# Kernel optimization log

Hardware: AMD Instinct MI355X
Metric: run time of the kernel (lower is better)

## Reference

```python
import jax, jax.numpy as jnp
import numpy as np

BLOCKSIZE = 128
NUM_EXPERTS = 16
TOP_K = 6
HIDDEN = 2048
INTER = 1408
TOKENS = 4096
N_BLK_H = HIDDEN // BLOCKSIZE   # 16
N_BLK_I = -(-INTER // BLOCKSIZE)  # 11 (ceil)


def setup_inputs() -> dict:
    key = jax.random.key(0)
    ks = jax.random.split(key, 8)
    x = jax.random.normal(ks[0], (TOKENS, HIDDEN), dtype=jnp.float32)
    selected_experts = jax.random.randint(ks[1], (TOKENS, TOP_K), 0, NUM_EXPERTS)
    # quantized-style weights + per-block scales (dequant = w * repeat(s, blocksize))
    w0 = jax.random.normal(ks[2], (NUM_EXPERTS, INTER, HIDDEN), dtype=jnp.float32) * 0.02
    s0 = jax.random.uniform(ks[3], (NUM_EXPERTS, INTER, N_BLK_H), dtype=jnp.float32, minval=0.5, maxval=1.5)
    w1 = jax.random.normal(ks[4], (NUM_EXPERTS, INTER, HIDDEN), dtype=jnp.float32) * 0.02
    s1 = jax.random.uniform(ks[5], (NUM_EXPERTS, INTER, N_BLK_H), dtype=jnp.float32, minval=0.5, maxval=1.5)
    w2 = jax.random.normal(ks[6], (NUM_EXPERTS, HIDDEN, INTER), dtype=jnp.float32) * 0.02
    s2 = jax.random.uniform(ks[7], (NUM_EXPERTS, HIDDEN, N_BLK_I), dtype=jnp.float32, minval=0.5, maxval=1.5)
    return {"x": x, "selected_experts": selected_experts,
            "w0": w0, "s0": s0, "w1": w1, "s1": s1, "w2": w2, "s2": s2}


def _dequant(w, s):
    # w: [E, O, I], s: [E, O, ceil(I/bs)] -> broadcast each scale over its block
    s_full = jnp.repeat(s, BLOCKSIZE, axis=-1)[..., : w.shape[-1]]
    return w * s_full


def reference(x, selected_experts, w0, s0, w1, s1, w2, s2):
    # Dequantize block-quantized expert weights.
    W0 = _dequant(w0, s0)  # gate proj [E, I, H]
    W1 = _dequant(w1, s1)  # up proj   [E, I, H]
    W2 = _dequant(w2, s2)  # down proj [E, H, I]
    # Original loops token x slot, calling expert(x[i]). Equivalent batched form:
    # compute every expert on every token, then gather by (token, slot) index.
    gate = jnp.einsum('th,eih->eti', x, W0)            # [E, T, I]
    up = jnp.einsum('th,eih->eti', x, W1)              # [E, T, I]
    act = jax.nn.silu(gate) * up                       # [E, T, I]
    all_out = jnp.einsum('eti,ehi->eth', act, W2)      # [E, T, H]
    tok = jnp.arange(x.shape[0])[:, None]              # [T, 1]
    out = all_out[selected_experts, tok]               # [T, K, H]
    return out
```

## Files before the change

kernel.cpp:

```cpp
#include <hip/hip_runtime.h>
#include <stdint.h>

#define TOKENS 4096
#define HIDDEN 2048
#define INTER  1408
#define NEXP   16
#define TOPK   6
#define NPAIR  (TOKENS*TOPK)
#define BM     128
#define MAXTILES (NPAIR/BM + NEXP)
#define MAXT2  (NPAIR/256 + NEXP)
#define NT1    (INTER/128)
#define NT2    (HIDDEN/128)
#define NT2W   (HIDDEN/256)

typedef __attribute__((ext_vector_type(8))) short bf16x8;
typedef __attribute__((ext_vector_type(4))) float f32x4;

__device__ __forceinline__ short f2bf(float f){
  union { float f; uint32_t u; } v; v.f = f;
  uint32_t r = (v.u + 0x7FFFu + ((v.u >> 16) & 1u)) >> 16;
  return (short)(r & 0xFFFFu);
}

__device__ __forceinline__ void gld16(const void* g, const void* l){
  __builtin_amdgcn_global_load_lds((const __attribute__((address_space(1))) void*)g,
                                   (__attribute__((address_space(3))) void*)l, 16, 0, 0);
}

__device__ __forceinline__ f32x4 ntld4(const float* p){
  return __builtin_nontemporal_load((const f32x4*)p);
}

#define SB() __builtin_amdgcn_sched_barrier(0)
#define BAR() __builtin_amdgcn_s_barrier()
#define WAITV(n) asm volatile("s_waitcnt vmcnt(" #n ")" ::: "memory")
#define WAITL() asm volatile("s_waitcnt lgkmcnt(0)" ::: "memory")


__global__ void k_xcast(const float* __restrict__ x, short* __restrict__ xb){
  int i = (blockIdx.x * 256 + threadIdx.x) * 8;
  f32x4 a = ntld4(x + i);
  f32x4 b = ntld4(x + i + 4);
  bf16x8 o;
  #pragma unroll
  for (int j = 0; j < 4; ++j){ o[j] = f2bf(a[j]); o[4+j] = f2bf(b[j]); }
  *(bf16x8*)(xb + i) = o;
}

__global__ void k_deq01(const float* __restrict__ w0, const float* __restrict__ s0,
                        const float* __restrict__ w1, const float* __restrict__ s1,
                        short* __restrict__ o0, short* __restrict__ o1){
  int row = blockIdx.x;
  const float* w; const float* s; short* o;
  if (row < NEXP * INTER){ w = w0; s = s0; o = o0; }
  else { row -= NEXP * INTER; w = w1; s = s1; o = o1; }
  const size_t base = (size_t)row * HIDDEN;
  const int c = threadIdx.x * 8;
  float sc = s[(size_t)row * (HIDDEN/128) + (c >> 7)];
  f32x4 a = ntld4(w + base + c);
  f32x4 b = ntld4(w + base + c + 4);
  bf16x8 h;
  #pragma unroll
  for (int j = 0; j < 4; ++j){ h[j] = f2bf(a[j] * sc); h[4+j] = f2bf(b[j] * sc); }
  *(bf16x8*)(o + base + c) = h;
}

__global__ void k_deqw2(const float* __restrict__ w2, const float* __restrict__ s2,
                        short* __restrict__ o){
  const int total = NEXP * HIDDEN * (INTER / 8);
  for (int gi = blockIdx.x * 256 + threadIdx.x; gi < total; gi += gridDim.x * 256){
    int row = gi / (INTER / 8);
    int c = (gi - row * (INTER / 8)) * 8;
    const size_t base = (size_t)row * INTER;
    float sc = s2[(size_t)row * 11 + (c >> 7)];
    f32x4 a = ntld4(w2 + base + c);
    f32x4 b = ntld4(w2 + base + c + 4);
    bf16x8 h;
    #pragma unroll
    for (int j = 0; j < 4; ++j){ h[j] = f2bf(a[j] * sc); h[4+j] = f2bf(b[j] * sc); }
    *(bf16x8*)(o + base + c) = h;
  }
}

__global__ void k_dequant(const float* __restrict__ w, const float* __restrict__ s,
                          short* __restrict__ o, int rowlen, int nblk){
  const int row = blockIdx.x;
  const size_t base = (size_t)row * rowlen;
  for (int c = threadIdx.x * 8; c < rowlen; c += blockDim.x * 8){
    float sc = s[(size_t)row * nblk + (c >> 7)];
    f32x4 a = *(const f32x4*)(w + base + c);
    f32x4 b = *(const f32x4*)(w + base + c + 4);
    bf16x8 h;
    #pragma unroll
    for (int j = 0; j < 4; ++j){ h[j] = f2bf(a[j] * sc); h[4+j] = f2bf(b[j] * sc); }
    *(bf16x8*)(o + base + c) = h;
  }
}

__global__ void k_count(const int* __restrict__ sel, int* __restrict__ cnt){
  int p = blockIdx.x * 256 + threadIdx.x;
  if (p < NPAIR) atomicAdd(&cnt[sel[p]], 1);
}

__global__ void k_scan(const int* __restrict__ cnt, int* __restrict__ offsets,
                       int2* __restrict__ tiles, int* __restrict__ ntiles,
                       int2* __restrict__ tiles2, int* __restrict__ ntiles2){
  if (threadIdx.x != 0) return;
  int off = 0, nt = 0, nt2 = 0;
  for (int e = 0; e < NEXP; ++e){
    offsets[e] = off;
    int c = cnt[e];
    for (int m = 0; m < c; m += BM){
      int rows = c - m; if (rows > BM) rows = BM;
      tiles[nt++] = make_int2(off + m, (e << 16) | rows);
    }
    for (int m = 0; m < c; m += 256){
      int rows = c - m; if (rows > 256) rows = 256;
      tiles2[nt2++] = make_int2(off + m, (e << 16) | rows);
    }
    off += c;
  }
  offsets[NEXP] = off;
  *ntiles = nt;
  *ntiles2 = nt2;
}

__global__ void k_scatter(const int* __restrict__ sel, const int* __restrict__ offsets,
                          int* __restrict__ cursor, int* __restrict__ pair_tk){
  int p = blockIdx.x * 256 + threadIdx.x;
  if (p >= NPAIR) return;
  int e = sel[p];
  int pos = offsets[e] + atomicAdd(&cursor[e], 1);
  pair_tk[pos] = (p / TOPK) * 8 + (p % TOPK);
}


__global__ __launch_bounds__(512) void k_g1(
    const short* __restrict__ xb,
    const short* __restrict__ w0b, const short* __restrict__ w1b,
    const int2* __restrict__ tiles2, const int* __restrict__ ntiles2,
    const int* __restrict__ pair_tk, short* __restrict__ act)
{
  const int nwg = MAXT2 * NT1;
  const int orig = (int)(blockIdx.y * MAXT2 + blockIdx.x);
  const int wg = (orig & 7) * (nwg >> 3) + (orig >> 3);
  const int tx = wg % MAXT2, ty = wg / MAXT2;
  if (tx >= *ntiles2) return;
  const int2 td = tiles2[tx];
  const int mstart = td.x;
  const int e  = td.y >> 16;
  const int vr = td.y & 0xFFFF;

  __shared__ short lA[4][8192];
  __shared__ short lB[4][8192];

  const int tid = threadIdx.x, w = tid >> 6, lane = tid & 63;

  const short* pA[2]; const short* pB[2]; int sg8[2];
  #pragma unroll
  for (int i = 0; i < 2; ++i){
    int s = (w * 2 + i) * 64 + lane;
    int r = s >> 2, j = (s & 3) ^ ((s >> 3) & 3);
    sg8[i] = s * 8;
    int p = mstart + r; if (p >= NPAIR) p = NPAIR - 1;
    pA[i] = xb + (size_t)(pair_tk[p] >> 3) * HIDDEN + j * 8;
    int G = r >> 4, srow = (G >> 1) * 16 + (r & 15);
    const short* wsrc = (G & 1) ? w1b : w0b;
    pB[i] = wsrc + ((size_t)e * INTER + (size_t)ty * 128 + srow) * HIDDEN + j * 8;
  }
  auto stage = [&](int slot, int ko){
    #pragma unroll
    for (int i = 0; i < 2; ++i) gld16(pA[i] + ko, &lA[slot][sg8[i]]);
    #pragma unroll
    for (int i = 0; i < 2; ++i) gld16(pB[i] + ko, &lB[slot][sg8[i]]);
  };

  f32x4 acc[4][8];
  #pragma unroll
  for (int i = 0; i < 4; ++i)
    #pragma unroll
    for (int j = 0; j < 8; ++j) acc[i][j] = (f32x4)0.f;

  const int cc = lane & 15, ks = lane >> 4;
  const int sx = (ks ^ ((cc >> 1) & 3)) * 8;
  const int wm = w >> 1, wn = w & 1;
  int arow[4], brow[8];
  #pragma unroll
  for (int mf = 0; mf < 4; ++mf) arow[mf] = (wm * 64 + mf * 16 + cc) * 32;
  #pragma unroll
  for (int nf = 0; nf < 8; ++nf) brow[nf] = (wn * 128 + nf * 16 + cc) * 32;

  stage(0, 0); stage(1, 32); stage(2, 64); stage(3, 96);

  #pragma unroll 1
  for (int t = 0; t < 32; ++t){
    const int b = t & 1;
    if (t == 0)      { WAITV(12); }
    else if (t < 31) { WAITV(8);  }
    else             { WAITV(4);  }
    SB(); BAR(); SB();
    {
      bf16x8 a0[4], bb[8];
      #pragma unroll
      for (int mf = 0; mf < 4; ++mf) a0[mf] = *(const bf16x8*)&lA[b*2][arow[mf] + sx];
      #pragma unroll
      for (int nf = 0; nf < 8; ++nf) bb[nf] = *(const bf16x8*)&lB[b*2][brow[nf] + sx];
      if (t >= 1 && t + 1 < 32) stage(((t+1)&1)*2 + 1, (t+1)*64 + 32);
      WAITL(); SB();
      __builtin_amdgcn_s_setprio(1);
      #pragma unroll
      for (int nf = 0; nf < 8; ++nf)
        #pragma unroll
        for (int mf = 0; mf < 4; ++mf)
          acc[mf][nf] = __builtin_amdgcn_mfma_f32_16x16x32_bf16(a0[mf], bb[nf], acc[mf][nf], 0, 0, 0);
      __builtin_amdgcn_s_setprio(0);
      SB(); BAR(); SB();
    }
    if (t < 31) { WAITV(8); } else { WAITV(0); }
    SB(); BAR(); SB();
    {
      bf16x8 a0[4], bb[8];
      #pragma unroll
      for (int mf = 0; mf < 4; ++mf) a0[mf] = *(const bf16x8*)&lA[b*2+1][arow[mf] + sx];
      #pragma unroll
      for (int nf = 0; nf < 8; ++nf) bb[nf] = *(const bf16x8*)&lB[b*2+1][brow[nf] + sx];
      if (t + 2 < 32) stage(b*2, (t+2)*64);
      WAITL(); SB();
      __builtin_amdgcn_s_setprio(1);
      #pragma unroll
      for (int nf = 0; nf < 8; ++nf)
        #pragma unroll
        for (int mf = 0; mf < 4; ++mf)
          acc[mf][nf] = __builtin_amdgcn_mfma_f32_16x16x32_bf16(a0[mf], bb[nf], acc[mf][nf], 0, 0, 0);
      __builtin_amdgcn_s_setprio(0);
      SB(); BAR(); SB();
    }
  }

  #pragma unroll
  for (int mf = 0; mf < 4; ++mf){
    #pragma unroll
    for (int j = 0; j < 4; ++j){
      int row = wm * 64 + mf * 16 + ks * 4 + j;
      if (row < vr){
        short* ar = act + (size_t)(mstart + row) * INTER + (size_t)ty * 128 + cc;
        #pragma unroll
        for (int q = 0; q < 4; ++q){
          float g = acc[mf][2*q][j], u = acc[mf][2*q+1][j];
          float a = g / (1.f + __expf(-g)) * u;
          ar[(wn * 4 + q) * 16] = f2bf(a);
        }
      }
    }
  }
}

__global__ __launch_bounds__(512) void k_g2(
    const short* __restrict__ act, const short* __restrict__ w2b,
    const int2* __restrict__ tiles2, const int* __restrict__ ntiles2,
    const int* __restrict__ pair_tk, float* __restrict__ out)
{
  const int nwg = MAXT2 * NT2W;
  const int orig = (int)(blockIdx.y * MAXT2 + blockIdx.x);
  const int wg = (orig & 7) * (nwg >> 3) + (orig >> 3);
  const int tx = wg % MAXT2, ty = wg / MAXT2;
  if (tx >= *ntiles2) return;
  const int2 td = tiles2[tx];
  const int mstart = td.x;
  const int e  = td.y >> 16;
  const int vr = td.y & 0xFFFF;

  __shared__ short lA[4][8192];
  __shared__ short lB[4][8192];

  const int tid = threadIdx.x, w = tid >> 6, lane = tid & 63;

  const short* pA[2]; const short* pB[2]; int sg8[2];
  #pragma unroll
  for (int i = 0; i < 2; ++i){
    int s = (w * 2 + i) * 64 + lane;
    int r = s >> 2, j = (s & 3) ^ ((s >> 3) & 3);
    sg8[i] = s * 8;
    int p = mstart + r; if (p >= NPAIR) p = NPAIR - 1;
    pA[i] = act + (size_t)p * INTER + j * 8;
    pB[i] = w2b + ((size_t)e * HIDDEN + (size_t)ty * 256 + r) * INTER + j * 8;
  }
  auto stage = [&](int slot, int ko){
    #pragma unroll
    for (int i = 0; i < 2; ++i) gld16(pA[i] + ko, &lA[slot][sg8[i]]);
    #pragma unroll
    for (int i = 0; i < 2; ++i) gld16(pB[i] + ko, &lB[slot][sg8[i]]);
  };

  f32x4 acc[4][8];
  #pragma unroll
  for (int i = 0; i < 4; ++i)
    #pragma unroll
    for (int j = 0; j < 8; ++j) acc[i][j] = (f32x4)0.f;

  const int cc = lane & 15, ks = lane >> 4;
  const int sx = (ks ^ ((cc >> 1) & 3)) * 8;
  const int wm = w >> 1, wn = w & 1;
  int arow[4], brow[8];
  #pragma unroll
  for (int mf = 0; mf < 4; ++mf) arow[mf] = (wm * 64 + mf * 16 + cc) * 32;
  #pragma unroll
  for (int nf = 0; nf < 8; ++nf) brow[nf] = (wn * 128 + nf * 16 + cc) * 32;

  stage(0, 0); stage(1, 32); stage(2, 64); stage(3, 96);

  #pragma unroll 1
  for (int t = 0; t < 22; ++t){
    const int b = t & 1;
    if (t == 0)      { WAITV(12); }
    else if (t < 21) { WAITV(8);  }
    else             { WAITV(4);  }
    SB(); BAR(); SB();
    {
      bf16x8 a0[4], bb[8];
      #pragma unroll
      for (int mf = 0; mf < 4; ++mf) a0[mf] = *(const bf16x8*)&lA[b*2][arow[mf] + sx];
      #pragma unroll
      for (int nf = 0; nf < 8; ++nf) bb[nf] = *(const bf16x8*)&lB[b*2][brow[nf] + sx];
      if (t >= 1 && t + 1 < 22) stage(((t+1)&1)*2 + 1, (t+1)*64 + 32);
      WAITL(); SB();
      __builtin_amdgcn_s_setprio(1);
      #pragma unroll
      for (int nf = 0; nf < 8; ++nf)
        #pragma unroll
        for (int mf = 0; mf < 4; ++mf)
          acc[mf][nf] = __builtin_amdgcn_mfma_f32_16x16x32_bf16(a0[mf], bb[nf], acc[mf][nf], 0, 0, 0);
      __builtin_amdgcn_s_setprio(0);
      SB(); BAR(); SB();
    }
    if (t < 21) { WAITV(8); } else { WAITV(0); }
    SB(); BAR(); SB();
    {
      bf16x8 a0[4], bb[8];
      #pragma unroll
      for (int mf = 0; mf < 4; ++mf) a0[mf] = *(const bf16x8*)&lA[b*2+1][arow[mf] + sx];
      #pragma unroll
      for (int nf = 0; nf < 8; ++nf) bb[nf] = *(const bf16x8*)&lB[b*2+1][brow[nf] + sx];
      if (t + 2 < 22) stage(b*2, (t+2)*64);
      WAITL(); SB();
      __builtin_amdgcn_s_setprio(1);
      #pragma unroll
      for (int nf = 0; nf < 8; ++nf)
        #pragma unroll
        for (int mf = 0; mf < 4; ++mf)
          acc[mf][nf] = __builtin_amdgcn_mfma_f32_16x16x32_bf16(a0[mf], bb[nf], acc[mf][nf], 0, 0, 0);
      __builtin_amdgcn_s_setprio(0);
      SB(); BAR(); SB();
    }
  }

  #pragma unroll
  for (int mf = 0; mf < 4; ++mf){
    #pragma unroll
    for (int j = 0; j < 4; ++j){
      int row = wm * 64 + mf * 16 + ks * 4 + j;
      if (row < vr){
        int ptk = pair_tk[mstart + row];
        float* orow = out + ((size_t)(ptk >> 3) * TOPK + (ptk & 7)) * HIDDEN
                      + (size_t)ty * 256 + wn * 128 + cc;
        #pragma unroll
        for (int nf = 0; nf < 8; ++nf)
          orow[nf * 16] = acc[mf][nf][j];
      }
    }
  }
}


__global__ __launch_bounds__(256) void k_gemm1(
    const short* __restrict__ xb,
    const float* __restrict__ w0, const float* __restrict__ s0,
    const float* __restrict__ w1, const float* __restrict__ s1,
    const int2* __restrict__ tiles, const int* __restrict__ ntiles,
    const int* __restrict__ pair_tk, short* __restrict__ act)
{
  if ((int)blockIdx.x >= *ntiles) return;
  const int2 td = tiles[blockIdx.x];
  const int mstart = td.x;
  const int e  = td.y >> 16;
  const int vr = td.y & 0xFFFF;
  const int tid = threadIdx.x;
  const int lane = tid & 63;

  __shared__ short lA[BM * 32];
  __shared__ short lB0[BM * 40];
  __shared__ short lB1[BM * 40];

  const int r0 = tid >> 2, r1 = 64 + (tid >> 2);
  const int seg = tid & 3;
  int p0 = mstart + r0; if (p0 >= NPAIR) p0 = NPAIR - 1;
  int p1 = mstart + r1; if (p1 >= NPAIR) p1 = NPAIR - 1;
  const short* arow0 = xb + (size_t)(pair_tk[p0] >> 3) * HIDDEN + (seg ^ ((r0 >> 1) & 3)) * 8;
  const short* arow1 = xb + (size_t)(pair_tk[p1] >> 3) * HIDDEN + (seg ^ ((r1 >> 1) & 3)) * 8;
  const short* ldsA0 = &lA[tid * 8];
  const short* ldsA1 = &lA[2048 + tid * 8];

  const int brow = tid >> 1, half = tid & 1;
  const int gbrow = blockIdx.y * BM + brow;
  const float* w0row = w0 + ((size_t)e * INTER + gbrow) * HIDDEN + half * 16;
  const float* w1row = w1 + ((size_t)e * INTER + gbrow) * HIDDEN + half * 16;
  const float* s0row = s0 + ((size_t)e * INTER + gbrow) * (HIDDEN / 128);
  const float* s1row = s1 + ((size_t)e * INTER + gbrow) * (HIDDEN / 128);
  short* lb0w = &lB0[brow * 40 + half * 16];
  short* lb1w = &lB1[brow * 40 + half * 16];

  f32x4 acc0[4][4], acc1[4][4];
  #pragma unroll
  for (int i = 0; i < 4; ++i)
    #pragma unroll
    for (int j = 0; j < 4; ++j){ acc0[i][j] = (f32x4)0.f; acc1[i][j] = (f32x4)0.f; }

  const int wm = tid >> 7, wn = (tid >> 6) & 1;
  const int cc = lane & 15, ks = lane >> 4;

  for (int kt = 0; kt < HIDDEN / 32; ++kt){
    gld16(arow0 + kt * 32, ldsA0);
    gld16(arow1 + kt * 32, ldsA1);
    {
      float sc = s0row[kt >> 2];
      const float* g = w0row + kt * 32;
      f32x4 q0 = *(const f32x4*)g,       q1 = *(const f32x4*)(g + 4),
            q2 = *(const f32x4*)(g + 8), q3 = *(const f32x4*)(g + 12);
      bf16x8 h0, h1;
      #pragma unroll
      for (int i = 0; i < 4; ++i){
        h0[i] = f2bf(q0[i] * sc); h0[4 + i] = f2bf(q1[i] * sc);
        h1[i] = f2bf(q2[i] * sc); h1[4 + i] = f2bf(q3[i] * sc);
      }
      *(bf16x8*)lb0w = h0; *(bf16x8*)(lb0w + 8) = h1;
    }
    {
      float sc = s1row[kt >> 2];
      const float* g = w1row + kt * 32;
      f32x4 q0 = *(const f32x4*)g,       q1 = *(const f32x4*)(g + 4),
            q2 = *(const f32x4*)(g + 8), q3 = *(const f32x4*)(g + 12);
      bf16x8 h0, h1;
      #pragma unroll
      for (int i = 0; i < 4; ++i){
        h0[i] = f2bf(q0[i] * sc); h0[4 + i] = f2bf(q1[i] * sc);
        h1[i] = f2bf(q2[i] * sc); h1[4 + i] = f2bf(q3[i] * sc);
      }
      *(bf16x8*)lb1w = h0; *(bf16x8*)(lb1w + 8) = h1;
    }
    __syncthreads();

    bf16x8 af[4];
    #pragma unroll
    for (int mf = 0; mf < 4; ++mf){
      int row = wm * 64 + mf * 16 + cc;
      af[mf] = *(const bf16x8*)&lA[row * 32 + ((ks ^ ((row >> 1) & 3)) * 8)];
    }
    #pragma unroll
    for (int nf = 0; nf < 4; ++nf){
      int rb = wn * 64 + nf * 16 + cc;
      bf16x8 b0 = *(const bf16x8*)&lB0[rb * 40 + ks * 8];
      bf16x8 b1 = *(const bf16x8*)&lB1[rb * 40 + ks * 8];
      #pragma unroll
      for (int mf = 0; mf < 4; ++mf)
        acc0[mf][nf] = __builtin_amdgcn_mfma_f32_16x16x32_bf16(af[mf], b0, acc0[mf][nf], 0, 0, 0);
      #pragma unroll
      for (int mf = 0; mf < 4; ++mf)
        acc1[mf][nf] = __builtin_amdgcn_mfma_f32_16x16x32_bf16(af[mf], b1, acc1[mf][nf], 0, 0, 0);
    }
    __syncthreads();
  }

  const int rbase = wm * 64 + (lane >> 4) * 4;
  #pragma unroll
  for (int mf = 0; mf < 4; ++mf){
    #pragma unroll
    for (int j = 0; j < 4; ++j){
      int row = rbase + mf * 16 + j;
      if (row < vr){
        short* ar = act + (size_t)(mstart + row) * INTER + blockIdx.y * BM + wn * 64 + cc;
        #pragma unroll
        for (int nf = 0; nf < 4; ++nf){
          float g = acc0[mf][nf][j], u = acc1[mf][nf][j];
          float a = g / (1.f + __expf(-g)) * u;
          ar[nf * 16] = f2bf(a);
        }
      }
    }
  }
}

__global__ __launch_bounds__(256) void k_gemm2(
    const short* __restrict__ act,
    const float* __restrict__ w2, const float* __restrict__ s2,
    const int2* __restrict__ tiles, const int* __restrict__ ntiles,
    const int* __restrict__ pair_tk, float* __restrict__ out)
{
  if ((int)blockIdx.x >= *ntiles) return;
  const int2 td = tiles[blockIdx.x];
  const int mstart = td.x;
  const int e  = td.y >> 16;
  const int vr = td.y & 0xFFFF;
  const int tid = threadIdx.x;
  const int lane = tid & 63;

  __shared__ short lA[BM * 32];
  __shared__ short lB[BM * 40];

  const int r0 = tid >> 2, r1 = 64 + (tid >> 2);
  const int seg = tid & 3;
  int p0 = mstart + r0; if (p0 >= NPAIR) p0 = NPAIR - 1;
  int p1 = mstart + r1; if (p1 >= NPAIR) p1 = NPAIR - 1;
  const short* arow0 = act + (size_t)p0 * INTER + (seg ^ ((r0 >> 1) & 3)) * 8;
  const short* arow1 = act + (size_t)p1 * INTER + (seg ^ ((r1 >> 1) & 3)) * 8;
  const short* ldsA0 = &lA[tid * 8];
  const short* ldsA1 = &lA[2048 + tid * 8];

  const int brow = tid >> 1, half = tid & 1;
  const int gbrow = blockIdx.y * BM + brow;
  const float* w2row = w2 + ((size_t)e * HIDDEN + gbrow) * INTER + half * 16;
  const float* s2row = s2 + ((size_t)e * HIDDEN + gbrow) * 11;
  short* lbw = &lB[brow * 40 + half * 16];

  f32x4 acc[4][4];
  #pragma unroll
  for (int i = 0; i < 4; ++i)
    #pragma unroll
    for (int j = 0; j < 4; ++j) acc[i][j] = (f32x4)0.f;

  const int wm = tid >> 7, wn = (tid >> 6) & 1;
  const int cc = lane & 15, ks = lane >> 4;

  for (int kt = 0; kt < INTER / 32; ++kt){
    gld16(arow0 + kt * 32, ldsA0);
    gld16(arow1 + kt * 32, ldsA1);
    {
      float sc = s2row[kt >> 2];
      const float* g = w2row + kt * 32;
      f32x4 q0 = *(const f32x4*)g,       q1 = *(const f32x4*)(g + 4),
            q2 = *(const f32x4*)(g + 8), q3 = *(const f32x4*)(g + 12);
      bf16x8 h0, h1;
      #pragma unroll
      for (int i = 0; i < 4; ++i){
        h0[i] = f2bf(q0[i] * sc); h0[4 + i] = f2bf(q1[i] * sc);
        h1[i] = f2bf(q2[i] * sc); h1[4 + i] = f2bf(q3[i] * sc);
      }
      *(bf16x8*)lbw = h0; *(bf16x8*)(lbw + 8) = h1;
    }
    __syncthreads();

    bf16x8 af[4];
    #pragma unroll
    for (int mf = 0; mf < 4; ++mf){
      int row = wm * 64 + mf * 16 + cc;
      af[mf] = *(const bf16x8*)&lA[row * 32 + ((ks ^ ((row >> 1) & 3)) * 8)];
    }
    #pragma unroll
    for (int nf = 0; nf < 4; ++nf){
      int rb = wn * 64 + nf * 16 + cc;
      bf16x8 b = *(const bf16x8*)&lB[rb * 40 + ks * 8];
      #pragma unroll
      for (int mf = 0; mf < 4; ++mf)
        acc[mf][nf] = __builtin_amdgcn_mfma_f32_16x16x32_bf16(af[mf], b, acc[mf][nf], 0, 0, 0);
    }
    __syncthreads();
  }

  const int rbase = wm * 64 + (lane >> 4) * 4;
  #pragma unroll
  for (int mf = 0; mf < 4; ++mf){
    #pragma unroll
    for (int j = 0; j < 4; ++j){
      int row = rbase + mf * 16 + j;
      if (row < vr){
        int ptk = pair_tk[mstart + row];
        float* orow = out + ((size_t)(ptk >> 3) * TOPK + (ptk & 7)) * HIDDEN
                      + blockIdx.y * BM + wn * 64 + cc;
        #pragma unroll
        for (int nf = 0; nf < 4; ++nf)
          orow[nf * 16] = acc[mf][nf][j];
      }
    }
  }
}


extern "C" void kernel_launch(void* const* d_in, const int* in_sizes, int n_in,
                              void* d_out, int out_size, void* d_ws, size_t ws_size,
                              hipStream_t stream)
{
  const float* x  = (const float*)d_in[0];
  const int*   sel= (const int*)  d_in[1];
  const float* w0 = (const float*)d_in[2];
  const float* s0 = (const float*)d_in[3];
  const float* w1 = (const float*)d_in[4];
  const float* s1 = (const float*)d_in[5];
  const float* w2 = (const float*)d_in[6];
  const float* s2 = (const float*)d_in[7];
  float* out = (float*)d_out;

  char* ws = (char*)d_ws;
  size_t o = 0;
  auto alloc = [&](size_t n){ size_t r = o; o = (o + n + 255) & ~(size_t)255; return r; };
  int*  cnt     = (int*) (ws + alloc(64));
  int*  cursor  = (int*) (ws + alloc(64));
  int*  offsets = (int*) (ws + alloc(68));
  int*  ntiles  = (int*) (ws + alloc(4));
  int*  ntiles2 = (int*) (ws + alloc(4));
  int2* tiles   = (int2*)(ws + alloc(MAXTILES * 8));
  int2* tiles2  = (int2*)(ws + alloc(MAXT2 * 8));
  int*  pair_tk = (int*) (ws + alloc((size_t)NPAIR * 4));
  short* xb     = (short*)(ws + alloc((size_t)TOKENS * HIDDEN * 2));
  short* act    = (short*)(ws + alloc((size_t)NPAIR * INTER * 2));
  const size_t WSZ = (size_t)NEXP * INTER * HIDDEN * 2;
  short* w0b    = (short*)(ws + alloc(WSZ));
  short* w1b    = (short*)(ws + alloc(WSZ));
  short* w2b    = (short*)(ws + alloc(WSZ));
  const bool predeq = (ws_size >= o);
  (void)in_sizes; (void)n_in; (void)out_size;

  hipMemsetAsync(ws, 0, 512, stream);

  k_xcast  <<<(TOKENS * HIDDEN) / (256 * 8), 256, 0, stream>>>(x, xb);
  k_count  <<<(NPAIR + 255) / 256, 256, 0, stream>>>(sel, cnt);
  k_scan   <<<1, 64, 0, stream>>>(cnt, offsets, tiles, ntiles, tiles2, ntiles2);
  k_scatter<<<(NPAIR + 255) / 256, 256, 0, stream>>>(sel, offsets, cursor, pair_tk);

  if (predeq){
    k_deq01<<<2 * NEXP * INTER, 256, 0, stream>>>(w0, s0, w1, s1, w0b, w1b);
    k_g1<<<dim3(MAXT2, NT1), 512, 0, stream>>>(xb, w0b, w1b,
                                               tiles2, ntiles2, pair_tk, act);
    k_deqw2<<<2048, 256, 0, stream>>>(w2, s2, w2b);
    k_g2<<<dim3(MAXT2, NT2W), 512, 0, stream>>>(act, w2b,
                                                tiles2, ntiles2, pair_tk, out);
  } else {
    k_gemm1<<<dim3(MAXTILES, NT1), 256, 0, stream>>>(xb, w0, s0, w1, s1,
                                                     tiles, ntiles, pair_tk, act);
    k_gemm2<<<dim3(MAXTILES, NT2), 256, 0, stream>>>(act, w2, s2,
                                                     tiles, ntiles, pair_tk, out);
  }
}
```

Measured before the change: 818.4 us.

## Switch GEMMs to 32x32x16 MFMA and fuse w2 dequant into first GEMM

Both grouped GEMM kernels move from 16x16x32 MFMA tiles to 32x32x16 MFMA with 16-float accumulators, and the LDS read addressing, swizzle and epilogue row mapping are adjusted to match. The gate/up interleave granularity in the B staging changes from 16 to 32 rows so the silu*up pairing lines up with the larger fragments. The separate w2 dequantization kernel is removed, and its grid-stride loop is appended to the tail of k_g1, so every workgroup, including early-exit ones, dequantizes part of w2 after its GEMM work. This saves a launch and lets memory-bound dequant overlap with compute-bound tiles, but it lengthens k_g1 and its tail and changes register pressure.

```diff
diff --git a/kernel.cpp b/kernel.cpp
--- a/kernel.cpp
+++ b/kernel.cpp
@@ -14,8 +14,9 @@
 #define NT2    (HIDDEN/128)
 #define NT2W   (HIDDEN/256)
 
-typedef __attribute__((ext_vector_type(8))) short bf16x8;
-typedef __attribute__((ext_vector_type(4))) float f32x4;
+typedef __attribute__((ext_vector_type(8)))  short bf16x8;
+typedef __attribute__((ext_vector_type(4)))  float f32x4;
+typedef __attribute__((ext_vector_type(16))) float f32x16;
 
 __device__ __forceinline__ short f2bf(float f){
   union { float f; uint32_t u; } v; v.f = f;
@@ -66,23 +67,6 @@
   *(bf16x8*)(o + base + c) = h;
 }
 
-__global__ void k_deqw2(const float* __restrict__ w2, const float* __restrict__ s2,
-                        short* __restrict__ o){
-  const int total = NEXP * HIDDEN * (INTER / 8);
-  for (int gi = blockIdx.x * 256 + threadIdx.x; gi < total; gi += gridDim.x * 256){
-    int row = gi / (INTER / 8);
-    int c = (gi - row * (INTER / 8)) * 8;
-    const size_t base = (size_t)row * INTER;
-    float sc = s2[(size_t)row * 11 + (c >> 7)];
-    f32x4 a = ntld4(w2 + base + c);
-    f32x4 b = ntld4(w2 + base + c + 4);
-    bf16x8 h;
-    #pragma unroll
-    for (int j = 0; j < 4; ++j){ h[j] = f2bf(a[j] * sc); h[4+j] = f2bf(b[j] * sc); }
-    *(bf16x8*)(o + base + c) = h;
-  }
-}
-
 __global__ void k_dequant(const float* __restrict__ w, const float* __restrict__ s,
                           short* __restrict__ o, int rowlen, int nblk){
   const int row = blockIdx.x;
@@ -140,118 +124,136 @@
     const short* __restrict__ xb,
     const short* __restrict__ w0b, const short* __restrict__ w1b,
     const int2* __restrict__ tiles2, const int* __restrict__ ntiles2,
-    const int* __restrict__ pair_tk, short* __restrict__ act)
+    const int* __restrict__ pair_tk, short* __restrict__ act,
+    const float* __restrict__ w2, const float* __restrict__ s2,
+    short* __restrict__ w2b)
 {
   const int nwg = MAXT2 * NT1;
   const int orig = (int)(blockIdx.y * MAXT2 + blockIdx.x);
   const int wg = (orig & 7) * (nwg >> 3) + (orig >> 3);
   const int tx = wg % MAXT2, ty = wg / MAXT2;
-  if (tx >= *ntiles2) return;
-  const int2 td = tiles2[tx];
-  const int mstart = td.x;
-  const int e  = td.y >> 16;
-  const int vr = td.y & 0xFFFF;
+  const int tid = threadIdx.x, w = tid >> 6, lane = tid & 63;
 
   __shared__ short lA[4][8192];
   __shared__ short lB[4][8192];
 
-  const int tid = threadIdx.x, w = tid >> 6, lane = tid & 63;
-
-  const short* pA[2]; const short* pB[2]; int sg8[2];
-  #pragma unroll
-  for (int i = 0; i < 2; ++i){
-    int s = (w * 2 + i) * 64 + lane;
-    int r = s >> 2, j = (s & 3) ^ ((s >> 3) & 3);
-    sg8[i] = s * 8;
-    int p = mstart + r; if (p >= NPAIR) p = NPAIR - 1;
-    pA[i] = xb + (size_t)(pair_tk[p] >> 3) * HIDDEN + j * 8;
-    int G = r >> 4, srow = (G >> 1) * 16 + (r & 15);
-    const short* wsrc = (G & 1) ? w1b : w0b;
-    pB[i] = wsrc + ((size_t)e * INTER + (size_t)ty * 128 + srow) * HIDDEN + j * 8;
-  }
-  auto stage = [&](int slot, int ko){
-    #pragma unroll
-    for (int i = 0; i < 2; ++i) gld16(pA[i] + ko, &lA[slot][sg8[i]]);
-    #pragma unroll
-    for (int i = 0; i < 2; ++i) gld16(pB[i] + ko, &lB[slot][sg8[i]]);
-  };
-
-  f32x4 acc[4][8];
-  #pragma unroll
-  for (int i = 0; i < 4; ++i)
-    #pragma unroll
-    for (int j = 0; j < 8; ++j) acc[i][j] = (f32x4)0.f;
-
-  const int cc = lane & 15, ks = lane >> 4;
-  const int sx = (ks ^ ((cc >> 1) & 3)) * 8;
-  const int wm = w >> 1, wn = w & 1;
-  int arow[4], brow[8];
-  #pragma unroll
-  for (int mf = 0; mf < 4; ++mf) arow[mf] = (wm * 64 + mf * 16 + cc) * 32;
-  #pragma unroll
-  for (int nf = 0; nf < 8; ++nf) brow[nf] = (wn * 128 + nf * 16 + cc) * 32;
-
-  stage(0, 0); stage(1, 32); stage(2, 64); stage(3, 96);
-
-  #pragma unroll 1
-  for (int t = 0; t < 32; ++t){
-    const int b = t & 1;
-    if (t == 0)      { WAITV(12); }
-    else if (t < 31) { WAITV(8);  }
-    else             { WAITV(4);  }
-    SB(); BAR(); SB();
-    {
-      bf16x8 a0[4], bb[8];
-      #pragma unroll
-      for (int mf = 0; mf < 4; ++mf) a0[mf] = *(const bf16x8*)&lA[b*2][arow[mf] + sx];
-      #pragma unroll
-      for (int nf = 0; nf < 8; ++nf) bb[nf] = *(const bf16x8*)&lB[b*2][brow[nf] + sx];
-      if (t >= 1 && t + 1 < 32) stage(((t+1)&1)*2 + 1, (t+1)*64 + 32);
-      WAITL(); SB();
-      __builtin_amdgcn_s_setprio(1);
-      #pragma unroll
-      for (int nf = 0; nf < 8; ++nf)
-        #pragma unroll
-        for (int mf = 0; mf < 4; ++mf)
-          acc[mf][nf] = __builtin_amdgcn_mfma_f32_16x16x32_bf16(a0[mf], bb[nf], acc[mf][nf], 0, 0, 0);
-      __builtin_amdgcn_s_setprio(0);
-      SB(); BAR(); SB();
-    }
-    if (t < 31) { WAITV(8); } else { WAITV(0); }
-    SB(); BAR(); SB();
-    {
-      bf16x8 a0[4], bb[8];
-      #pragma unroll
-      for (int mf = 0; mf < 4; ++mf) a0[mf] = *(const bf16x8*)&lA[b*2+1][arow[mf] + sx];
-      #pragma unroll
-      for (int nf = 0; nf < 8; ++nf) bb[nf] = *(const bf16x8*)&lB[b*2+1][brow[nf] + sx];
-      if (t + 2 < 32) stage(b*2, (t+2)*64);
-      WAITL(); SB();
-      __builtin_amdgcn_s_setprio(1);
-      #pragma unroll
-      for (int nf = 0; nf < 8; ++nf)
-        #pragma unroll
-        for (int mf = 0; mf < 4; ++mf)
-          acc[mf][nf] = __builtin_amdgcn_mfma_f32_16x16x32_bf16(a0[mf], bb[nf], acc[mf][nf], 0, 0, 0);
-      __builtin_amdgcn_s_setprio(0);
-      SB(); BAR(); SB();
-    }
-  }
-
-  #pragma unroll
-  for (int mf = 0; mf < 4; ++mf){
-    #pragma unroll
-    for (int j = 0; j < 4; ++j){
-      int row = wm * 64 + mf * 16 + ks * 4 + j;
-      if (row < vr){
-        short* ar = act + (size_t)(mstart + row) * INTER + (size_t)ty * 128 + cc;
-        #pragma unroll
-        for (int q = 0; q < 4; ++q){
-          float g = acc[mf][2*q][j], u = acc[mf][2*q+1][j];
-          float a = g / (1.f + __expf(-g)) * u;
-          ar[(wn * 4 + q) * 16] = f2bf(a);
+  if (tx < *ntiles2){
+    const int2 td = tiles2[tx];
+    const int mstart = td.x;
+    const int e  = td.y >> 16;
+    const int vr = td.y & 0xFFFF;
+
+    const short* pA[2]; const short* pB[2]; int sg8[2];
+    #pragma unroll
+    for (int i = 0; i < 2; ++i){
+      int s = (w * 2 + i) * 64 + lane;
+      int r = s >> 2, j = (s & 3) ^ ((s >> 3) & 3);
+      sg8[i] = s * 8;
+      int p = mstart + r; if (p >= NPAIR) p = NPAIR - 1;
+      pA[i] = xb + (size_t)(pair_tk[p] >> 3) * HIDDEN + j * 8;
+      int G = r >> 5, srow = (G >> 1) * 32 + (r & 31);
+      const short* wsrc = (G & 1) ? w1b : w0b;
+      pB[i] = wsrc + ((size_t)e * INTER + (size_t)ty * 128 + srow) * HIDDEN + j * 8;
+    }
+    auto stage = [&](int slot, int ko){
+      #pragma unroll
+      for (int i = 0; i < 2; ++i) gld16(pA[i] + ko, &lA[slot][sg8[i]]);
+      #pragma unroll
+      for (int i = 0; i < 2; ++i) gld16(pB[i] + ko, &lB[slot][sg8[i]]);
+    };
+
+    f32x16 acc[2][4];
+    #pragma unroll
+    for (int i = 0; i < 2; ++i)
+      #pragma unroll
+      for (int j = 0; j < 4; ++j) acc[i][j] = (f32x16)0.f;
+
+    const int c32 = lane & 31, kg = lane >> 5;
+    const int wm = w >> 1, wn = w & 1;
+    int arow[2], axor[2], brow[4], bxor[4];
+    #pragma unroll
+    for (int mf = 0; mf < 2; ++mf){
+      int r = wm * 64 + mf * 32 + c32;
+      arow[mf] = r * 32; axor[mf] = (r >> 1) & 3;
+    }
+    #pragma unroll
+    for (int nf = 0; nf < 4; ++nf){
+      int r = wn * 128 + nf * 32 + c32;
+      brow[nf] = r * 32; bxor[nf] = (r >> 1) & 3;
+    }
+
+    stage(0, 0); stage(1, 32); stage(2, 64); stage(3, 96);
+
+    #pragma unroll 1
+    for (int t = 0; t < 32; ++t){
+      const int b = t & 1;
+      #pragma unroll
+      for (int h = 0; h < 2; ++h){
+        if (t == 0 && h == 0)      { WAITV(12); }
+        else if (t < 31)           { WAITV(8);  }
+        else if (h == 0)           { WAITV(4);  }
+        else                       { WAITV(0);  }
+        SB(); BAR(); SB();
+        const short* A = lA[b*2 + h];
+        const short* B = lB[b*2 + h];
+        bf16x8 av[2][2], bv[4][2];
+        #pragma unroll
+        for (int mf = 0; mf < 2; ++mf)
+          #pragma unroll
+          for (int k2 = 0; k2 < 2; ++k2)
+            av[mf][k2] = *(const bf16x8*)&A[arow[mf] + (((k2*2+kg) ^ axor[mf]) * 8)];
+        #pragma unroll
+        for (int nf = 0; nf < 4; ++nf)
+          #pragma unroll
+          for (int k2 = 0; k2 < 2; ++k2)
+            bv[nf][k2] = *(const bf16x8*)&B[brow[nf] + (((k2*2+kg) ^ bxor[nf]) * 8)];
+        if (h == 0){ if (t >= 1 && t + 1 < 32) stage(((t+1)&1)*2 + 1, (t+1)*64 + 32); }
+        else       { if (t + 2 < 32)           stage(b*2, (t+2)*64); }
+        WAITL(); SB();
+        __builtin_amdgcn_s_setprio(1);
+        #pragma unroll
+        for (int k2 = 0; k2 < 2; ++k2)
+          #pragma unroll
+          for (int nf = 0; nf < 4; ++nf)
+            #pragma unroll
+            for (int mf = 0; mf < 2; ++mf)
+              acc[mf][nf] = __builtin_amdgcn_mfma_f32_32x32x16_bf16(av[mf][k2], bv[nf][k2], acc[mf][nf], 0, 0, 0);
+        __builtin_amdgcn_s_setprio(0);
+        SB(); BAR(); SB();
+      }
+    }
+
+    #pragma unroll
+    for (int mf = 0; mf < 2; ++mf){
+      #pragma unroll
+      for (int r = 0; r < 16; ++r){
+        int row = wm * 64 + mf * 32 + (r & 3) + 8 * (r >> 2) + 4 * kg;
+        if (row < vr){
+          short* ar = act + (size_t)(mstart + row) * INTER + (size_t)ty * 128 + c32;
+          #pragma unroll
+          for (int t2 = 0; t2 < 2; ++t2){
+            float g = acc[mf][2*t2][r], u = acc[mf][2*t2+1][r];
+            float a = g / (1.f + __expf(-g)) * u;
+            ar[(wn * 2 + t2) * 32] = f2bf(a);
+          }
         }
       }
+    }
+  }
+
+  {
+    const int total = NEXP * HIDDEN * (INTER / 8);
+    for (int gi = orig * 512 + tid; gi < total; gi += nwg * 512){
+      int row = gi / (INTER / 8);
+      int c = (gi - row * (INTER / 8)) * 8;
+      const size_t base = (size_t)row * INTER;
+      float sc = s2[(size_t)row * 11 + (c >> 7)];
+      f32x4 a = ntld4(w2 + base + c);
+      f32x4 b = ntld4(w2 + base + c + 4);
+      bf16x8 h;
+      #pragma unroll
+      for (int j = 0; j < 4; ++j){ h[j] = f2bf(a[j] * sc); h[4+j] = f2bf(b[j] * sc); }
+      *(bf16x8*)(w2b + base + c) = h;
     }
   }
 }
@@ -293,80 +295,79 @@
     for (int i = 0; i < 2; ++i) gld16(pB[i] + ko, &lB[slot][sg8[i]]);
   };
 
-  f32x4 acc[4][8];
-  #pragma unroll
-  for (int i = 0; i < 4; ++i)
-    #pragma unroll
-    for (int j = 0; j < 8; ++j) acc[i][j] = (f32x4)0.f;
-
-  const int cc = lane & 15, ks = lane >> 4;
-  const int sx = (ks ^ ((cc >> 1) & 3)) * 8;
+  f32x16 acc[2][4];
+  #pragma unroll
+  for (int i = 0; i < 2; ++i)
+    #pragma unroll
+    for (int j = 0; j < 4; ++j) acc[i][j] = (f32x16)0.f;
+
+  const int c32 = lane & 31, kg = lane >> 5;
   const int wm = w >> 1, wn = w & 1;
-  int arow[4], brow[8];
-  #pragma unroll
-  for (int mf = 0; mf < 4; ++mf) arow[mf] = (wm * 64 + mf * 16 + cc) * 32;
-  #pragma unroll
-  for (int nf = 0; nf < 8; ++nf) brow[nf] = (wn * 128 + nf * 16 + cc) * 32;
+  int arow[2], axor[2], brow[4], bxor[4];
+  #pragma unroll
+  for (int mf = 0; mf < 2; ++mf){
+    int r = wm * 64 + mf * 32 + c32;
+    arow[mf] = r * 32; axor[mf] = (r >> 1) & 3;
+  }
+  #pragma unroll
+  for (int nf = 0; nf < 4; ++nf){
+    int r = wn * 128 + nf * 32 + c32;
+    brow[nf] = r * 32; bxor[nf] = (r >> 1) & 3;
+  }
 
   stage(0, 0); stage(1, 32); stage(2, 64); stage(3, 96);
 
   #pragma unroll 1
   for (int t = 0; t < 22; ++t){
     const int b = t & 1;
-    if (t == 0)      { WAITV(12); }
-    else if (t < 21) { WAITV(8);  }
-    else             { WAITV(4);  }
-    SB(); BAR(); SB();
-    {
-      bf16x8 a0[4], bb[8];
-      #pragma unroll
-      for (int mf = 0; mf < 4; ++mf) a0[mf] = *(const bf16x8*)&lA[b*2][arow[mf] + sx];
-      #pragma unroll
-      for (int nf = 0; nf < 8; ++nf) bb[nf] = *(const bf16x8*)&lB[b*2][brow[nf] + sx];
-      if (t >= 1 && t + 1 < 22) stage(((t+1)&1)*2 + 1, (t+1)*64 + 32);
+    #pragma unroll
+    for (int h = 0; h < 2; ++h){
+      if (t == 0 && h == 0)      { WAITV(12); }
+      else if (t < 21)           { WAITV(8);  }
+      else if (h == 0)           { WAITV(4);  }
+      else                       { WAITV(0);  }
+      SB(); BAR(); SB();
+      const short* A = lA[b*2 + h];
+      const short* B = lB[b*2 + h];
+      bf16x8 av[2][2], bv[4][2];
+      #pragma unroll
+      for (int mf = 0; mf < 2; ++mf)
+        #pragma unroll
+        for (int k2 = 0; k2 < 2; ++k2)
+          av[mf][k2] = *(const bf16x8*)&A[arow[mf] + (((k2*2+kg) ^ axor[mf]) * 8)];
+      #pragma unroll
+      for (int nf = 0; nf < 4; ++nf)
+        #pragma unroll
+        for (int k2 = 0; k2 < 2; ++k2)
+          bv[nf][k2] = *(const bf16x8*)&B[brow[nf] + (((k2*2+kg) ^ bxor[nf]) * 8)];
+      if (h == 0){ if (t >= 1 && t + 1 < 22) stage(((t+1)&1)*2 + 1, (t+1)*64 + 32); }
+      else       { if (t + 2 < 22)           stage(b*2, (t+2)*64); }
       WAITL(); SB();
       __builtin_amdgcn_s_setprio(1);
       #pragma unroll
-      for (int nf = 0; nf < 8; ++nf)
-        #pragma unroll
-        for (int mf = 0; mf < 4; ++mf)
-          acc[mf][nf] = __builtin_amdgcn_mfma_f32_16x16x32_bf16(a0[mf], bb[nf], acc[mf][nf], 0, 0, 0);
+      for (int k2 = 0; k2 < 2; ++k2)
+        #pragma unroll
+        for (int nf = 0; nf < 4; ++nf)
+          #pragma unroll
+          for (int mf = 0; mf < 2; ++mf)
+            acc[mf][nf] = __builtin_amdgcn_mfma_f32_32x32x16_bf16(av[mf][k2], bv[nf][k2], acc[mf][nf], 0, 0, 0);
       __builtin_amdgcn_s_setprio(0);
       SB(); BAR(); SB();
     }
-    if (t < 21) { WAITV(8); } else { WAITV(0); }
-    SB(); BAR(); SB();
-    {
-      bf16x8 a0[4], bb[8];
-      #pragma unroll
-      for (int mf = 0; mf < 4; ++mf) a0[mf] = *(const bf16x8*)&lA[b*2+1][arow[mf] + sx];
-      #pragma unroll
-      for (int nf = 0; nf < 8; ++nf) bb[nf] = *(const bf16x8*)&lB[b*2+1][brow[nf] + sx];
-      if (t + 2 < 22) stage(b*2, (t+2)*64);
-      WAITL(); SB();
-      __builtin_amdgcn_s_setprio(1);
-      #pragma unroll
-      for (int nf = 0; nf < 8; ++nf)
-        #pragma unroll
-        for (int mf = 0; mf < 4; ++mf)
-          acc[mf][nf] = __builtin_amdgcn_mfma_f32_16x16x32_bf16(a0[mf], bb[nf], acc[mf][nf], 0, 0, 0);
-      __builtin_amdgcn_s_setprio(0);
-      SB(); BAR(); SB();
-    }
-  }
-
-  #pragma unroll
-  for (int mf = 0; mf < 4; ++mf){
-    #pragma unroll
-    for (int j = 0; j < 4; ++j){
-      int row = wm * 64 + mf * 16 + ks * 4 + j;
+  }
+
+  #pragma unroll
+  for (int mf = 0; mf < 2; ++mf){
+    #pragma unroll
+    for (int r = 0; r < 16; ++r){
+      int row = wm * 64 + mf * 32 + (r & 3) + 8 * (r >> 2) + 4 * kg;
       if (row < vr){
         int ptk = pair_tk[mstart + row];
         float* orow = out + ((size_t)(ptk >> 3) * TOPK + (ptk & 7)) * HIDDEN
-                      + (size_t)ty * 256 + wn * 128 + cc;
-        #pragma unroll
-        for (int nf = 0; nf < 8; ++nf)
-          orow[nf * 16] = acc[mf][nf][j];
+                      + (size_t)ty * 256 + wn * 128 + c32;
+        #pragma unroll
+        for (int nf = 0; nf < 4; ++nf)
+          orow[nf * 32] = acc[mf][nf][r];
       }
     }
   }
@@ -629,8 +630,8 @@
   if (predeq){
     k_deq01<<<2 * NEXP * INTER, 256, 0, stream>>>(w0, s0, w1, s1, w0b, w1b);
     k_g1<<<dim3(MAXT2, NT1), 512, 0, stream>>>(xb, w0b, w1b,
-                                               tiles2, ntiles2, pair_tk, act);
-    k_deqw2<<<2048, 256, 0, stream>>>(w2, s2, w2b);
+                                               tiles2, ntiles2, pair_tk, act,
+                                               w2, s2, w2b);
     k_g2<<<dim3(MAXT2, NT2W), 512, 0, stream>>>(act, w2b,
                                                 tiles2, ntiles2, pair_tk, out);
   } else {
```

Result: slower. 863.3 us (+5.5%).

## Stage GEMM epilogues through LDS for coalesced stores and fuse x cast

Applied to the files above, without the earlier changes.

The epilogues of both grouped GEMMs now write accumulator fragments into shared memory first, then each wave stores whole rows contiguously (4-byte writes for the bf16 activations, 16-byte writes for the fp32 output). The old path issued scattered 2- and 4-byte strided stores. The x-to-bf16 cast is also folded into the w0/w1 dequant launch as extra blocks, removing one kernel launch. The cost is extra LDS traffic and barriers in the epilogue, and k_g2 needs two passes because its 256x256 fp32 tile does not fit in LDS at once.

```diff
diff --git a/kernel.cpp b/kernel.cpp
--- a/kernel.cpp
+++ b/kernel.cpp
@@ -38,20 +38,21 @@
 #define WAITL() asm volatile("s_waitcnt lgkmcnt(0)" ::: "memory")
 
 
-__global__ void k_xcast(const float* __restrict__ x, short* __restrict__ xb){
-  int i = (blockIdx.x * 256 + threadIdx.x) * 8;
-  f32x4 a = ntld4(x + i);
-  f32x4 b = ntld4(x + i + 4);
-  bf16x8 o;
-  #pragma unroll
-  for (int j = 0; j < 4; ++j){ o[j] = f2bf(a[j]); o[4+j] = f2bf(b[j]); }
-  *(bf16x8*)(xb + i) = o;
-}
-
-__global__ void k_deq01(const float* __restrict__ w0, const float* __restrict__ s0,
-                        const float* __restrict__ w1, const float* __restrict__ s1,
-                        short* __restrict__ o0, short* __restrict__ o1){
+__global__ void k_deq01x(const float* __restrict__ x, short* __restrict__ xb,
+                         const float* __restrict__ w0, const float* __restrict__ s0,
+                         const float* __restrict__ w1, const float* __restrict__ s1,
+                         short* __restrict__ o0, short* __restrict__ o1){
   int row = blockIdx.x;
+  if (row >= 2 * NEXP * INTER){
+    int i = ((row - 2 * NEXP * INTER) * 256 + threadIdx.x) * 8;
+    f32x4 a = ntld4(x + i);
+    f32x4 b = ntld4(x + i + 4);
+    bf16x8 o;
+    #pragma unroll
+    for (int j = 0; j < 4; ++j){ o[j] = f2bf(a[j]); o[4+j] = f2bf(b[j]); }
+    *(bf16x8*)(xb + i) = o;
+    return;
+  }
   const float* w; const float* s; short* o;
   if (row < NEXP * INTER){ w = w0; s = s0; o = o0; }
   else { row -= NEXP * INTER; w = w1; s = s1; o = o1; }
@@ -83,19 +84,14 @@
   }
 }
 
-__global__ void k_dequant(const float* __restrict__ w, const float* __restrict__ s,
-                          short* __restrict__ o, int rowlen, int nblk){
-  const int row = blockIdx.x;
-  const size_t base = (size_t)row * rowlen;
-  for (int c = threadIdx.x * 8; c < rowlen; c += blockDim.x * 8){
-    float sc = s[(size_t)row * nblk + (c >> 7)];
-    f32x4 a = *(const f32x4*)(w + base + c);
-    f32x4 b = *(const f32x4*)(w + base + c + 4);
-    bf16x8 h;
-    #pragma unroll
-    for (int j = 0; j < 4; ++j){ h[j] = f2bf(a[j] * sc); h[4+j] = f2bf(b[j] * sc); }
-    *(bf16x8*)(o + base + c) = h;
-  }
+__global__ void k_xcast(const float* __restrict__ x, short* __restrict__ xb){
+  int i = (blockIdx.x * 256 + threadIdx.x) * 8;
+  f32x4 a = ntld4(x + i);
+  f32x4 b = ntld4(x + i + 4);
+  bf16x8 o;
+  #pragma unroll
+  for (int j = 0; j < 4; ++j){ o[j] = f2bf(a[j]); o[4+j] = f2bf(b[j]); }
+  *(bf16x8*)(xb + i) = o;
 }
 
 __global__ void k_count(const int* __restrict__ sel, int* __restrict__ cnt){
@@ -152,8 +148,9 @@
   const int e  = td.y >> 16;
   const int vr = td.y & 0xFFFF;
 
-  __shared__ short lA[4][8192];
-  __shared__ short lB[4][8192];
+  __shared__ short lmem[8][8192];
+  short (*lA)[8192] = lmem;
+  short (*lB)[8192] = lmem + 4;
 
   const int tid = threadIdx.x, w = tid >> 6, lane = tid & 63;
 
@@ -238,20 +235,28 @@
     }
   }
 
+  short* lT = (short*)lmem;
+  __syncthreads();
   #pragma unroll
   for (int mf = 0; mf < 4; ++mf){
     #pragma unroll
     for (int j = 0; j < 4; ++j){
       int row = wm * 64 + mf * 16 + ks * 4 + j;
-      if (row < vr){
-        short* ar = act + (size_t)(mstart + row) * INTER + (size_t)ty * 128 + cc;
-        #pragma unroll
-        for (int q = 0; q < 4; ++q){
-          float g = acc[mf][2*q][j], u = acc[mf][2*q+1][j];
-          float a = g / (1.f + __expf(-g)) * u;
-          ar[(wn * 4 + q) * 16] = f2bf(a);
-        }
-      }
+      #pragma unroll
+      for (int q = 0; q < 4; ++q){
+        float g = acc[mf][2*q][j], u = acc[mf][2*q+1][j];
+        float a = g / (1.f + __expf(-g)) * u;
+        lT[row * 128 + (wn * 4 + q) * 16 + cc] = f2bf(a);
+      }
+    }
+  }
+  __syncthreads();
+  #pragma unroll 1
+  for (int rr = 0; rr < 32; ++rr){
+    int row = w * 32 + rr;
+    if (row < vr){
+      uint32_t v = *(const uint32_t*)&lT[row * 128 + lane * 2];
+      *(uint32_t*)&act[(size_t)(mstart + row) * INTER + (size_t)ty * 128 + lane * 2] = v;
     }
   }
 }
@@ -271,8 +276,9 @@
   const int e  = td.y >> 16;
   const int vr = td.y & 0xFFFF;
 
-  __shared__ short lA[4][8192];
-  __shared__ short lB[4][8192];
+  __shared__ short lmem[8][8192];
+  short (*lA)[8192] = lmem;
+  short (*lB)[8192] = lmem + 4;
 
   const int tid = threadIdx.x, w = tid >> 6, lane = tid & 63;
 
@@ -355,18 +361,34 @@
     }
   }
 
-  #pragma unroll
-  for (int mf = 0; mf < 4; ++mf){
-    #pragma unroll
-    for (int j = 0; j < 4; ++j){
-      int row = wm * 64 + mf * 16 + ks * 4 + j;
+  float* lT = (float*)lmem;
+  #pragma unroll 1
+  for (int p = 0; p < 2; ++p){
+    __syncthreads();
+    if ((wm >> 1) == p){
+      int rb = (wm & 1) * 64;
+      #pragma unroll
+      for (int mf = 0; mf < 4; ++mf){
+        #pragma unroll
+        for (int j = 0; j < 4; ++j){
+          int prow = rb + mf * 16 + ks * 4 + j;
+          #pragma unroll
+          for (int nf = 0; nf < 8; ++nf)
+            lT[prow * 256 + wn * 128 + nf * 16 + cc] = acc[mf][nf][j];
+        }
+      }
+    }
+    __syncthreads();
+    #pragma unroll 1
+    for (int rr = 0; rr < 16; ++rr){
+      int prow = w * 16 + rr;
+      int row = p * 128 + prow;
       if (row < vr){
         int ptk = pair_tk[mstart + row];
         float* orow = out + ((size_t)(ptk >> 3) * TOPK + (ptk & 7)) * HIDDEN
-                      + (size_t)ty * 256 + wn * 128 + cc;
-        #pragma unroll
-        for (int nf = 0; nf < 8; ++nf)
-          orow[nf * 16] = acc[mf][nf][j];
+                      + (size_t)ty * 256;
+        f32x4 v = *(const f32x4*)&lT[prow * 256 + lane * 4];
+        *(f32x4*)&orow[lane * 4] = v;
       }
     }
   }
@@ -621,19 +643,20 @@
 
   hipMemsetAsync(ws, 0, 512, stream);
 
-  k_xcast  <<<(TOKENS * HIDDEN) / (256 * 8), 256, 0, stream>>>(x, xb);
   k_count  <<<(NPAIR + 255) / 256, 256, 0, stream>>>(sel, cnt);
   k_scan   <<<1, 64, 0, stream>>>(cnt, offsets, tiles, ntiles, tiles2, ntiles2);
   k_scatter<<<(NPAIR + 255) / 256, 256, 0, stream>>>(sel, offsets, cursor, pair_tk);
 
   if (predeq){
-    k_deq01<<<2 * NEXP * INTER, 256, 0, stream>>>(w0, s0, w1, s1, w0b, w1b);
+    k_deq01x<<<2 * NEXP * INTER + (TOKENS * HIDDEN) / (256 * 8), 256, 0, stream>>>(
+        x, xb, w0, s0, w1, s1, w0b, w1b);
     k_g1<<<dim3(MAXT2, NT1), 512, 0, stream>>>(xb, w0b, w1b,
                                                tiles2, ntiles2, pair_tk, act);
     k_deqw2<<<2048, 256, 0, stream>>>(w2, s2, w2b);
     k_g2<<<dim3(MAXT2, NT2W), 512, 0, stream>>>(act, w2b,
                                                 tiles2, ntiles2, pair_tk, out);
   } else {
+    k_xcast  <<<(TOKENS * HIDDEN) / (256 * 8), 256, 0, stream>>>(x, xb);
     k_gemm1<<<dim3(MAXTILES, NT1), 256, 0, stream>>>(xb, w0, s0, w1, s1,
                                                      tiles, ntiles, pair_tk, act);
     k_gemm2<<<dim3(MAXTILES, NT2), 256, 0, stream>>>(act, w2, s2,
```

Result: no change. 822.9 us (+0.6%).
